# Kernel tuning notes

Hardware: AMD Instinct MI355X
Metric: run time of the kernel (lower is better)

Reference implementation:

```python
import jax, jax.numpy as jnp
import numpy as np

N = 262144        # number of rows (mesh nodes)
E = 2_000_000     # random off-diagonal pairs (symmetrized)
F = 4             # n_feature (columns of b)
RTOL = 1e-5
ATOL = 0.0
MAXITER = 100


def setup_inputs() -> dict:
    rng = np.random.default_rng(0)
    r = rng.integers(0, N, E)
    c = rng.integers(0, N, E)
    w = (rng.random(E) + 0.1).astype(np.float32)
    # symmetric diagonally-dominant matrix: Laplacian(w) + I  (SPD)
    row = np.concatenate([r, c, np.arange(N)]).astype(np.int32)
    col = np.concatenate([c, r, np.arange(N)]).astype(np.int32)
    deg = np.zeros(N, np.float32)
    np.add.at(deg, r, w)
    np.add.at(deg, c, w)
    vals = np.concatenate([-w, -w, deg + 1.0]).astype(np.float32)
    key = jax.random.key(0)
    b = jax.random.normal(key, (N, F), dtype=jnp.float32)
    return {
        "values": jnp.asarray(vals),
        "b": b,
        "row": jnp.asarray(row),
        "col": jnp.asarray(col),
    }


def _cg(values, row, col, rhs):
    """Batched CG solve of A x = rhs where A is COO (row, col, values).

    batch_solve=True semantics: the [n, f] unknown is treated as one long
    vector; dot products reduce over all n*f elements (as in the wrapped
    scipy LinearOperator of size (n*f, n*f)).
    """
    n = rhs.shape[0]

    def spmv(v):  # v: [n, f] -> [n, f]
        return jax.ops.segment_sum(values[:, None] * v[col], row, num_segments=n)

    bnorm = jnp.sqrt(jnp.sum(rhs * rhs))
    tol = jnp.maximum(RTOL * bnorm, ATOL)

    x0 = jnp.zeros_like(rhs)
    r0 = rhs  # b - A @ 0
    state = (x0, r0, r0, jnp.sum(r0 * r0), jnp.int32(0))

    def cond(s):
        _, _, _, rho, k = s
        return (jnp.sqrt(rho) > tol) & (k < MAXITER)

    def body(s):
        x, r, p, rho, k = s
        q = spmv(p)
        alpha = rho / jnp.sum(p * q)
        x = x + alpha * p
        r = r - alpha * q
        rho_new = jnp.sum(r * r)
        p = r + (rho_new / rho) * p
        return (x, r, p, rho_new, k + 1)

    x, _, _, _, _ = jax.lax.while_loop(cond, body, state)
    return x


def reference(values, b, row, col):
    return _cg(values, row, col, b)
```

## Files before the change

kernel.cpp:

```cpp
#include <hip/hip_runtime.h>

#define NT 1024
#define NB 256
#define MAXIT 100
#define RTOL_F 1e-5f

typedef float f4 __attribute__((ext_vector_type(4)));

__device__ __forceinline__ unsigned long long pk2(float a, float b) {
    return ((unsigned long long)__float_as_uint(b) << 32) | (unsigned long long)__float_as_uint(a);
}

__device__ __forceinline__ void ld16_cc(const f4* a, f4& d) {
    asm volatile("global_load_dwordx4 %0, %1, off sc0 sc1" : "=v"(d) : "v"(a));
}
__device__ __forceinline__ void wait16x8(f4& a, f4& b, f4& c, f4& d,
                                         f4& e, f4& f, f4& g, f4& h) {
    asm volatile("s_waitcnt vmcnt(0)"
                 : "+v"(a), "+v"(b), "+v"(c), "+v"(d),
                   "+v"(e), "+v"(f), "+v"(g), "+v"(h));
}
__device__ __forceinline__ void st16_cc(f4* a, f4 v) {
    asm volatile("global_store_dwordx4 %0, %1, off sc0 sc1" :: "v"(a), "v"(v) : "memory");
}

__device__ __forceinline__ void fbar(int* flags, int seq) {
    __syncthreads();
    if (threadIdx.x == 0)
        __hip_atomic_store(&flags[blockIdx.x], seq, __ATOMIC_RELAXED, __HIP_MEMORY_SCOPE_AGENT);
    if (threadIdx.x < 64) {
        const int b4 = threadIdx.x << 2;
        for (;;) {
            const int f0 = __hip_atomic_load(&flags[b4 + 0], __ATOMIC_RELAXED, __HIP_MEMORY_SCOPE_AGENT);
            const int f1 = __hip_atomic_load(&flags[b4 + 1], __ATOMIC_RELAXED, __HIP_MEMORY_SCOPE_AGENT);
            const int f2 = __hip_atomic_load(&flags[b4 + 2], __ATOMIC_RELAXED, __HIP_MEMORY_SCOPE_AGENT);
            const int f3 = __hip_atomic_load(&flags[b4 + 3], __ATOMIC_RELAXED, __HIP_MEMORY_SCOPE_AGENT);
            const bool ok = (f0 >= seq) && (f1 >= seq) && (f2 >= seq) && (f3 >= seq);
            if (__all(ok)) break;
            __builtin_amdgcn_s_sleep(1);
        }
    }
    __syncthreads();
}

__device__ __forceinline__ void fbar_heavy(int* flags, int seq) {
    __builtin_amdgcn_fence(__ATOMIC_RELEASE, "agent");
    fbar(flags, seq);
    __builtin_amdgcn_fence(__ATOMIC_ACQUIRE, "agent");
}

__device__ __forceinline__ float2 block_sum2_bcast(float a, float b, float* smf) {
#pragma unroll
    for (int o = 32; o > 0; o >>= 1) { a += __shfl_down(a, o); b += __shfl_down(b, o); }
    __syncthreads();
    const int w = threadIdx.x >> 6;
    if ((threadIdx.x & 63) == 0) { smf[w] = a; smf[16 + w] = b; }
    __syncthreads();
    float ra = 0.f, rb = 0.f;
#pragma unroll
    for (int i = 0; i < 16; ++i) { ra += smf[i]; rb += smf[16 + i]; }
    return make_float2(ra, rb);
}

__device__ __forceinline__ float2 sum_parts2(const unsigned long long* buf, float* smf) {
    float a = 0.f, b = 0.f;
    if (threadIdx.x < NB) {
        unsigned long long u = __hip_atomic_load(&buf[threadIdx.x], __ATOMIC_RELAXED,
                                                 __HIP_MEMORY_SCOPE_AGENT);
        a = __uint_as_float((unsigned)(u & 0xffffffffu));
        b = __uint_as_float((unsigned)(u >> 32));
    }
    return block_sum2_bcast(a, b, smf);
}

__device__ __forceinline__ int block_incl_scan(int v, int* smi) {
    const int t = threadIdx.x;
    smi[t] = v;
    __syncthreads();
    for (int off = 1; off < NT; off <<= 1) {
        int add = (t >= off) ? smi[t - off] : 0;
        __syncthreads();
        v += add;
        smi[t] = v;
        __syncthreads();
    }
    return v;
}

__device__ __forceinline__ f4 spmv_row(const long long* __restrict__ bp0, int J,
                                       const f4* __restrict__ rq) {
    f4 a4 = {0.f, 0.f, 0.f, 0.f};
    for (int j = 0; j < J; j += 8) {
        long long e[8];
#pragma unroll
        for (int u = 0; u < 8; ++u) e[u] = bp0[(j + u) * 64];
        f4 g0, g1, g2, g3, g4, g5, g6, g7;
        ld16_cc(rq + (int)(e[0] & 0xffffffffLL), g0);
        ld16_cc(rq + (int)(e[1] & 0xffffffffLL), g1);
        ld16_cc(rq + (int)(e[2] & 0xffffffffLL), g2);
        ld16_cc(rq + (int)(e[3] & 0xffffffffLL), g3);
        ld16_cc(rq + (int)(e[4] & 0xffffffffLL), g4);
        ld16_cc(rq + (int)(e[5] & 0xffffffffLL), g5);
        ld16_cc(rq + (int)(e[6] & 0xffffffffLL), g6);
        ld16_cc(rq + (int)(e[7] & 0xffffffffLL), g7);
        wait16x8(g0, g1, g2, g3, g4, g5, g6, g7);
        a4 += __int_as_float((int)(e[0] >> 32)) * g0;
        a4 += __int_as_float((int)(e[1] >> 32)) * g1;
        a4 += __int_as_float((int)(e[2] >> 32)) * g2;
        a4 += __int_as_float((int)(e[3] >> 32)) * g3;
        a4 += __int_as_float((int)(e[4] >> 32)) * g4;
        a4 += __int_as_float((int)(e[5] >> 32)) * g5;
        a4 += __int_as_float((int)(e[6] >> 32)) * g6;
        a4 += __int_as_float((int)(e[7] >> 32)) * g7;
    }
    return a4;
}

__global__ void __launch_bounds__(NT, 4)
cg_solver_kernel(const float* __restrict__ values,
                 const f4* __restrict__ bvec,
                 const int* __restrict__ rowi,
                 const int* __restrict__ coli,
                 f4* __restrict__ x,
                 f4* __restrict__ wA,
                 f4* __restrict__ wB,
                 int* __restrict__ counts,
                 int* __restrict__ ridx,
                 int* __restrict__ jarr,
                 int* __restrict__ soff,
                 unsigned long long* __restrict__ part,
                 int* __restrict__ flags,
                 long long* __restrict__ sell,
                 int n, int nnz, int nslice)
{
    const int t = threadIdx.x;
    const int tid = blockIdx.x * NT + t;
    const int nth = gridDim.x * NT;
    __shared__ int smi[NT];
    __shared__ float smf[32];
    int seq = 0;

    for (int i = tid; i < n; i += nth) { counts[i] = 0; ridx[i] = 0; }
    fbar_heavy(flags, ++seq);

    for (int e = tid; e < nnz; e += nth) atomicAdd(&counts[rowi[e]], 1);
    f4 rv = bvec[tid];
    st16_cc(&wB[tid], rv);
    fbar_heavy(flags, ++seq);

    for (int s = tid; s < nslice; s += nth) {
        const int rb = s << 6;
        int m = 0;
#pragma unroll 4
        for (int i = 0; i < 64; ++i) m = max(m, counts[rb + i]);
        jarr[s] = (m + 7) & ~7;
    }
    fbar_heavy(flags, ++seq);

    if (blockIdx.x == 0) {
        const int spt = (nslice + NT - 1) / NT;
        const int base = t * spt;
        int local = 0;
        for (int i = 0; i < spt; ++i) {
            int s = base + i;
            if (s < nslice) local += 64 * jarr[s];
        }
        int incl = block_incl_scan(local, smi);
        int run = incl - local;
        for (int i = 0; i < spt; ++i) {
            int s = base + i;
            if (s < nslice) { soff[s] = run; run += 64 * jarr[s]; }
        }
        if (t == NT - 1) soff[nslice] = incl;
    }
    fbar_heavy(flags, ++seq);

    {
        const int total = soff[nslice];
        for (int i = tid; i < total; i += nth) sell[i] = 0LL;
    }
    fbar_heavy(flags, ++seq);

    for (int e = tid; e < nnz; e += nth) {
        const int rr = rowi[e];
        const int i = atomicAdd(&ridx[rr], 1);
        const int pos = soff[rr >> 6] + (i << 6) + (rr & 63);
        sell[pos] = ((long long)__float_as_int(values[e]) << 32) | (unsigned int)coli[e];
    }
    fbar_heavy(flags, ++seq);

    const int wid = tid >> 6;
    const int lane = t & 63;
    const long long* __restrict__ bp0 = sell + soff[wid] + lane;
    const int J = jarr[wid];

    f4 pv = {0.f, 0.f, 0.f, 0.f};
    f4 sv = {0.f, 0.f, 0.f, 0.f};
    f4 zv = {0.f, 0.f, 0.f, 0.f};
    f4 xv = {0.f, 0.f, 0.f, 0.f};
    f4 wv;

    {
        wv = spmv_row(bp0, J, wB);
        st16_cc(&wA[tid], wv);
        float g_p = rv.x * rv.x + rv.y * rv.y + rv.z * rv.z + rv.w * rv.w;
        float d_p = rv.x * wv.x + rv.y * wv.y + rv.z * wv.z + rv.w * wv.w;
        float2 tot = block_sum2_bcast(g_p, d_p, smf);
        if (t == 0)
            __hip_atomic_store(&part[blockIdx.x], pk2(tot.x, tot.y), __ATOMIC_RELAXED, __HIP_MEMORY_SCOPE_AGENT);
    }
    fbar(flags, ++seq);

    float tol2 = 0.f;
    float rho_prev = 1.f;
    float alpha = 1.f;

    for (int k = 0;; ++k) {
        float2 rm = sum_parts2(part + (k & 1) * NB, smf);
        if (k == 0) tol2 = RTOL_F * RTOL_F * rm.x;
        if (!(rm.x > tol2 && k < MAXIT)) break;
        const float beta = (k == 0) ? 0.f : rm.x / rho_prev;
        alpha = rm.x / (rm.y - beta * rm.x / alpha);
        rho_prev = rm.x;

        const f4* wq = (k & 1) ? wB : wA;
        f4 qv = spmv_row(bp0, J, wq);

        zv = qv + beta * zv;
        sv = wv + beta * sv;
        pv = rv + beta * pv;
        xv = xv + alpha * pv;
        rv = rv - alpha * sv;
        wv = wv - alpha * zv;

        f4* wt = (k & 1) ? wA : wB;
        st16_cc(&wt[tid], wv);
        {
            float g_p = rv.x * rv.x + rv.y * rv.y + rv.z * rv.z + rv.w * rv.w;
            float d_p = rv.x * wv.x + rv.y * wv.y + rv.z * wv.z + rv.w * wv.w;
            float2 tot = block_sum2_bcast(g_p, d_p, smf);
            if (t == 0)
                __hip_atomic_store(&part[((k + 1) & 1) * NB + blockIdx.x], pk2(tot.x, tot.y),
                                   __ATOMIC_RELAXED, __HIP_MEMORY_SCOPE_AGENT);
        }
        fbar(flags, ++seq);
    }

    x[tid] = xv;
}

extern "C" void kernel_launch(void* const* d_in, const int* in_sizes, int n_in,
                              void* d_out, int out_size, void* d_ws, size_t ws_size,
                              hipStream_t stream) {
    const float* values = (const float*)d_in[0];
    const f4* bvec      = (const f4*)d_in[1];
    const int* rowi     = (const int*)d_in[2];
    const int* coli     = (const int*)d_in[3];
    const int nnz = in_sizes[0];
    const int n   = in_sizes[1] / 4;
    const int nslice = n / 64;

    char* ws = (char*)d_ws;
    size_t off = 0;
    auto alloc = [&](size_t bytes) -> void* {
        off = (off + 255) & ~(size_t)255;
        void* pp = ws + off;
        off += bytes;
        return pp;
    };
    int* flags   = (int*)alloc((size_t)NB * 4);
    f4* wA       = (f4*)alloc((size_t)n * 16);
    f4* wB       = (f4*)alloc((size_t)n * 16);
    unsigned long long* part = (unsigned long long*)alloc((size_t)2 * NB * 8);
    int* counts  = (int*)alloc((size_t)n * 4);
    int* ridx    = (int*)alloc((size_t)n * 4);
    int* jarr    = (int*)alloc((size_t)nslice * 4);
    int* soff    = (int*)alloc((size_t)(nslice + 1) * 4);
    off = (off + 255) & ~(size_t)255;
    long long* sell = (long long*)(ws + off);
    f4* x = (f4*)d_out;

    hipMemsetAsync(flags, 0, (size_t)NB * 4, stream);

    int n_ = n, nnz_ = nnz, nslice_ = nslice;
    void* args[] = {
        (void*)&values, (void*)&bvec, (void*)&rowi, (void*)&coli,
        (void*)&x, (void*)&wA, (void*)&wB,
        (void*)&counts, (void*)&ridx, (void*)&jarr, (void*)&soff,
        (void*)&part, (void*)&flags,
        (void*)&sell, (void*)&n_, (void*)&nnz_, (void*)&nslice_
    };
    hipLaunchCooperativeKernel((void*)cg_solver_kernel, dim3(NB), dim3(NT),
                               args, 0, stream);
}
```

Baseline: 1.856 ms.

## Sort rows by degree within blocks for SELL padding and prefetch SELL entries

Adds a per-block counting sort of rows by nonzero count (capped at 63), building a permutation so that each 64-row SELL slice groups rows of similar degree and pads less. The matrix columns, the right-hand side and the output are remapped through this permutation. The SpMV loop also software-prefetches the next group of eight packed entries while the gathers for the current group are in flight. The cost is an extra setup barrier, two permutation arrays and indirect accesses during setup.

```diff
diff --git a/kernel.cpp b/kernel.cpp
--- a/kernel.cpp
+++ b/kernel.cpp
@@ -90,28 +90,31 @@
 __device__ __forceinline__ f4 spmv_row(const long long* __restrict__ bp0, int J,
                                        const f4* __restrict__ rq) {
     f4 a4 = {0.f, 0.f, 0.f, 0.f};
+    long long e0 = bp0[0 * 64], e1 = bp0[1 * 64], e2 = bp0[2 * 64], e3 = bp0[3 * 64];
+    long long e4 = bp0[4 * 64], e5 = bp0[5 * 64], e6 = bp0[6 * 64], e7 = bp0[7 * 64];
     for (int j = 0; j < J; j += 8) {
-        long long e[8];
-#pragma unroll
-        for (int u = 0; u < 8; ++u) e[u] = bp0[(j + u) * 64];
         f4 g0, g1, g2, g3, g4, g5, g6, g7;
-        ld16_cc(rq + (int)(e[0] & 0xffffffffLL), g0);
-        ld16_cc(rq + (int)(e[1] & 0xffffffffLL), g1);
-        ld16_cc(rq + (int)(e[2] & 0xffffffffLL), g2);
-        ld16_cc(rq + (int)(e[3] & 0xffffffffLL), g3);
-        ld16_cc(rq + (int)(e[4] & 0xffffffffLL), g4);
-        ld16_cc(rq + (int)(e[5] & 0xffffffffLL), g5);
-        ld16_cc(rq + (int)(e[6] & 0xffffffffLL), g6);
-        ld16_cc(rq + (int)(e[7] & 0xffffffffLL), g7);
+        ld16_cc(rq + (int)(e0 & 0xffffffffLL), g0);
+        ld16_cc(rq + (int)(e1 & 0xffffffffLL), g1);
+        ld16_cc(rq + (int)(e2 & 0xffffffffLL), g2);
+        ld16_cc(rq + (int)(e3 & 0xffffffffLL), g3);
+        ld16_cc(rq + (int)(e4 & 0xffffffffLL), g4);
+        ld16_cc(rq + (int)(e5 & 0xffffffffLL), g5);
+        ld16_cc(rq + (int)(e6 & 0xffffffffLL), g6);
+        ld16_cc(rq + (int)(e7 & 0xffffffffLL), g7);
+        const long long* np = bp0 + (long long)min(j + 8, J - 8) * 64;
+        const long long f0 = np[0 * 64], f1 = np[1 * 64], f2 = np[2 * 64], f3 = np[3 * 64];
+        const long long f4_ = np[4 * 64], f5 = np[5 * 64], f6 = np[6 * 64], f7 = np[7 * 64];
         wait16x8(g0, g1, g2, g3, g4, g5, g6, g7);
-        a4 += __int_as_float((int)(e[0] >> 32)) * g0;
-        a4 += __int_as_float((int)(e[1] >> 32)) * g1;
-        a4 += __int_as_float((int)(e[2] >> 32)) * g2;
-        a4 += __int_as_float((int)(e[3] >> 32)) * g3;
-        a4 += __int_as_float((int)(e[4] >> 32)) * g4;
-        a4 += __int_as_float((int)(e[5] >> 32)) * g5;
-        a4 += __int_as_float((int)(e[6] >> 32)) * g6;
-        a4 += __int_as_float((int)(e[7] >> 32)) * g7;
+        a4 += __int_as_float((int)(e0 >> 32)) * g0;
+        a4 += __int_as_float((int)(e1 >> 32)) * g1;
+        a4 += __int_as_float((int)(e2 >> 32)) * g2;
+        a4 += __int_as_float((int)(e3 >> 32)) * g3;
+        a4 += __int_as_float((int)(e4 >> 32)) * g4;
+        a4 += __int_as_float((int)(e5 >> 32)) * g5;
+        a4 += __int_as_float((int)(e6 >> 32)) * g6;
+        a4 += __int_as_float((int)(e7 >> 32)) * g7;
+        e0 = f0; e1 = f1; e2 = f2; e3 = f3; e4 = f4_; e5 = f5; e6 = f6; e7 = f7;
     }
     return a4;
 }
@@ -126,6 +129,8 @@
                  f4* __restrict__ wB,
                  int* __restrict__ counts,
                  int* __restrict__ ridx,
+                 int* __restrict__ pos,
+                 int* __restrict__ rord,
                  int* __restrict__ jarr,
                  int* __restrict__ soff,
                  unsigned long long* __restrict__ part,
@@ -138,13 +143,36 @@
     const int nth = gridDim.x * NT;
     __shared__ int smi[NT];
     __shared__ float smf[32];
+    __shared__ int hist[64], binoff[64], bincur[64];
     int seq = 0;
 
     for (int i = tid; i < n; i += nth) { counts[i] = 0; ridx[i] = 0; }
     fbar_heavy(flags, ++seq);
 
     for (int e = tid; e < nnz; e += nth) atomicAdd(&counts[rowi[e]], 1);
-    f4 rv = bvec[tid];
+    fbar_heavy(flags, ++seq);
+
+    {
+        if (t < 64) hist[t] = 0;
+        __syncthreads();
+        const int d = min(counts[tid], 63);
+        atomicAdd(&hist[d], 1);
+        __syncthreads();
+        if (t == 0) {
+            int run = 0;
+            for (int i = 0; i < 64; ++i) { binoff[i] = run; run += hist[i]; }
+        }
+        __syncthreads();
+        if (t < 64) bincur[t] = 0;
+        __syncthreads();
+        const int lslot = binoff[d] + atomicAdd(&bincur[d], 1);
+        const int slot = blockIdx.x * NT + lslot;
+        pos[tid] = slot;
+        rord[slot] = tid;
+    }
+    __syncthreads();
+    const int orig = rord[tid];
+    f4 rv = bvec[orig];
     st16_cc(&wB[tid], rv);
     fbar_heavy(flags, ++seq);
 
@@ -152,7 +180,7 @@
         const int rb = s << 6;
         int m = 0;
 #pragma unroll 4
-        for (int i = 0; i < 64; ++i) m = max(m, counts[rb + i]);
+        for (int i = 0; i < 64; ++i) m = max(m, counts[rord[rb + i]]);
         jarr[s] = (m + 7) & ~7;
     }
     fbar_heavy(flags, ++seq);
@@ -184,8 +212,9 @@
     for (int e = tid; e < nnz; e += nth) {
         const int rr = rowi[e];
         const int i = atomicAdd(&ridx[rr], 1);
-        const int pos = soff[rr >> 6] + (i << 6) + (rr & 63);
-        sell[pos] = ((long long)__float_as_int(values[e]) << 32) | (unsigned int)coli[e];
+        const int slot = pos[rr];
+        const int p = soff[slot >> 6] + (i << 6) + (slot & 63);
+        sell[p] = ((long long)__float_as_int(values[e]) << 32) | (unsigned int)pos[coli[e]];
     }
     fbar_heavy(flags, ++seq);
 
@@ -246,7 +275,7 @@
         fbar(flags, ++seq);
     }
 
-    x[tid] = xv;
+    x[orig] = xv;
 }
 
 extern "C" void kernel_launch(void* const* d_in, const int* in_sizes, int n_in,
@@ -274,6 +303,8 @@
     unsigned long long* part = (unsigned long long*)alloc((size_t)2 * NB * 8);
     int* counts  = (int*)alloc((size_t)n * 4);
     int* ridx    = (int*)alloc((size_t)n * 4);
+    int* pos     = (int*)alloc((size_t)n * 4);
+    int* rord    = (int*)alloc((size_t)n * 4);
     int* jarr    = (int*)alloc((size_t)nslice * 4);
     int* soff    = (int*)alloc((size_t)(nslice + 1) * 4);
     off = (off + 255) & ~(size_t)255;
@@ -286,7 +317,8 @@
     void* args[] = {
         (void*)&values, (void*)&bvec, (void*)&rowi, (void*)&coli,
         (void*)&x, (void*)&wA, (void*)&wB,
-        (void*)&counts, (void*)&ridx, (void*)&jarr, (void*)&soff,
+        (void*)&counts, (void*)&ridx, (void*)&pos, (void*)&rord,
+        (void*)&jarr, (void*)&soff,
         (void*)&part, (void*)&flags,
         (void*)&sell, (void*)&n_, (void*)&nnz_, (void*)&nslice_
     };
```

After: 2.001 ms. 1.08x slower.
